# Performance work log

Hardware: AMD Instinct MI355X
Metric: run time of the kernel (lower is better)

## Reference

```python
import jax, jax.numpy as jnp
import numpy as np

D = 128        # node_state_dim
F = 10         # len(CHOSEN_CONNECTION_FEATURES)
N_IP = 20000
N_CONN = 100000
E = 200000
T = 3


def _seg_mean(vals, ids, n):
    s = jax.ops.segment_sum(vals, ids, num_segments=n)
    c = jax.ops.segment_sum(jnp.ones((vals.shape[0], 1), vals.dtype), ids, num_segments=n)
    return s / jnp.maximum(c, 1.0)


def _gru(x, h, kernel, rec_kernel, bias):
    # keras GRUCell, reset_after=True, gate order [z, r, hh]
    xm = x @ kernel + bias[0]
    hm = h @ rec_kernel + bias[1]
    xz, xr, xh = jnp.split(xm, 3, axis=-1)
    hz, hr, hh = jnp.split(hm, 3, axis=-1)
    z = jax.nn.sigmoid(xz + hz)
    r = jax.nn.sigmoid(xr + hr)
    hcand = jnp.tanh(xh + r * hh)
    return z * h + (1.0 - z) * hcand


def setup_inputs() -> dict:
    key = jax.random.key(0)
    ks = jax.random.split(key, 24)
    s = 0.02
    inp = {
        "feature_connection": jax.random.normal(ks[0], (N_CONN, F), jnp.float32),
        "src_ip_to_connection": jax.random.randint(ks[1], (E,), 0, N_IP, jnp.int32),
        "dst_ip_to_connection": jax.random.randint(ks[2], (E,), 0, N_CONN, jnp.int32),
        "src_connection_to_ip": jax.random.randint(ks[3], (E,), 0, N_CONN, jnp.int32),
        "dst_connection_to_ip": jax.random.randint(ks[4], (E,), 0, N_IP, jnp.int32),
        # message MLPs
        "W_m1": jax.random.normal(ks[5], (2 * D, D), jnp.float32) * s,
        "b_m1": jnp.zeros((D,), jnp.float32),
        "W_m2": jax.random.normal(ks[6], (2 * D, D), jnp.float32) * s,
        "b_m2": jnp.zeros((D,), jnp.float32),
        # GRU cells
        "gru_ip_k": jax.random.normal(ks[7], (D, 3 * D), jnp.float32) * s,
        "gru_ip_r": jax.random.normal(ks[8], (D, 3 * D), jnp.float32) * s,
        "gru_ip_b": jnp.zeros((2, 3 * D), jnp.float32),
        "gru_c_k": jax.random.normal(ks[9], (D, 3 * D), jnp.float32) * s,
        "gru_c_r": jax.random.normal(ks[10], (D, 3 * D), jnp.float32) * s,
        "gru_c_b": jnp.zeros((2, 3 * D), jnp.float32),
        # readout MLP
        "W_r1": jax.random.normal(ks[11], (D, 128), jnp.float32) * s,
        "b_r1": jnp.zeros((128,), jnp.float32),
        "W_r2": jax.random.normal(ks[12], (128, 64), jnp.float32) * s,
        "b_r2": jnp.zeros((64,), jnp.float32),
        "W_r3": jax.random.normal(ks[13], (64, 15), jnp.float32) * s,
        "b_r3": jnp.zeros((15,), jnp.float32),
    }
    return inp


def reference(feature_connection, src_ip_to_connection, dst_ip_to_connection,
              src_connection_to_ip, dst_connection_to_ip,
              W_m1, b_m1, W_m2, b_m2,
              gru_ip_k, gru_ip_r, gru_ip_b,
              gru_c_k, gru_c_r, gru_c_b,
              W_r1, b_r1, W_r2, b_r2, W_r3, b_r3):
    ip_state = jnp.ones((N_IP, D), jnp.float32)
    connection_state = jnp.concatenate(
        [feature_connection, jnp.zeros((N_CONN, D - F), jnp.float32)], axis=1)

    for _ in range(T):
        # ip -> connection messages
        nn_in = jnp.concatenate([ip_state[src_ip_to_connection],
                                 connection_state[dst_ip_to_connection]], axis=1)
        ip_message = jax.nn.relu(nn_in @ W_m1 + b_m1)            # [E, D]
        ip_mean = _seg_mean(ip_message, dst_ip_to_connection, N_CONN)
        # connection -> ip messages
        nn_in2 = jnp.concatenate([connection_state[src_connection_to_ip],
                                  ip_state[dst_connection_to_ip]], axis=1)
        conn_message = jax.nn.relu(nn_in2 @ W_m2 + b_m2)         # [E, D]
        conn_mean = _seg_mean(conn_message, dst_connection_to_ip, N_IP)
        # GRU updates
        ip_state = _gru(conn_mean, ip_state, gru_ip_k, gru_ip_r, gru_ip_b)
        connection_state = _gru(ip_mean, connection_state, gru_c_k, gru_c_r, gru_c_b)

    h = jax.nn.relu(connection_state @ W_r1 + b_r1)
    h = jax.nn.relu(h @ W_r2 + b_r2)
    return jax.nn.softmax(h @ W_r3 + b_r3, axis=-1)              # [N_CONN, 15]
```

## Files before the change

kernel.cpp:

```cpp
#include <hip/hip_runtime.h>
#include <math.h>

#define D 128
#define NF 10
#define N_IP 20000
#define N_CONN 100000
#define NE 200000
#define T_ROUNDS 3

typedef unsigned short u16;
using bf16x8 = __attribute__((ext_vector_type(8))) short;
using floatx4 = __attribute__((ext_vector_type(4))) float;

__device__ inline u16 f2bf(float f) {
  union { float f; unsigned u; } v; v.f = f;
  unsigned u = v.u;
  return (u16)((u + 0x7fffu + ((u >> 16) & 1u)) >> 16);
}
__device__ inline float bf2f(u16 h) {
  union { unsigned u; float f; } v; v.u = ((unsigned)h) << 16; return v.f;
}
__device__ __forceinline__ unsigned cvtpk(float lo, float hi) {
  unsigned r;
  asm("v_cvt_pk_bf16_f32 %0, %1, %2" : "=v"(r) : "v"(lo), "v"(hi));
  return r;
}

__device__ inline float fsigmoid(float s) { return 1.f / (1.f + __expf(-s)); }
__device__ inline float ftanh(float a) {
  a = fminf(fmaxf(a, -15.f), 15.f);
  float e = __expf(2.f * a);
  return (e - 1.f) / (e + 1.f);
}

__device__ __forceinline__ void gld16(const u16* g, u16* l) {
  __builtin_amdgcn_global_load_lds(
      (const __attribute__((address_space(1))) unsigned int*)g,
      (__attribute__((address_space(3))) unsigned int*)l, 16, 0, 0);
}

__global__ void k_setup(u16* __restrict__ ip_state, u16* __restrict__ conn_state,
                        const float* __restrict__ feat, int* __restrict__ cnt,
                        const float* __restrict__ gik, const float* __restrict__ gir,
                        const float* __restrict__ gck, const float* __restrict__ gcr,
                        const float* __restrict__ Wm1, const float* __restrict__ Wm2,
                        const float* __restrict__ Wr1, const float* __restrict__ Wr2,
                        u16* __restrict__ gikb, u16* __restrict__ girb,
                        u16* __restrict__ gckb, u16* __restrict__ gcrb,
                        u16* __restrict__ wm1b, u16* __restrict__ wm2b,
                        u16* __restrict__ wm1t, u16* __restrict__ wm2t,
                        u16* __restrict__ wr1b, u16* __restrict__ wr2b,
                        float* __restrict__ csum, int* __restrict__ gctr) {
  int i = blockIdx.x * blockDim.x + threadIdx.x;
  const int nip = N_IP * D;
  const int nstate = (N_IP + N_CONN) * D;
  if (i < nip) {
    ip_state[i] = 0x3F80;
  } else if (i < nstate) {
    int j = i - nip;
    int r = j >> 7, c = j & 127;
    conn_state[j] = (c < NF) ? f2bf(feat[r * NF + c]) : (u16)0;
  }
  if (i < N_CONN + N_IP) cnt[i] = 0;
  if (i < 2) gctr[i] = 0;
  if (i < 196608) {
    int m = i / 49152, r = i % 49152;
    const float* W = (m == 0) ? gik : (m == 1) ? gir : (m == 2) ? gck : gcr;
    u16* Wb = (m == 0) ? gikb : (m == 1) ? girb : (m == 2) ? gckb : gcrb;
    int col = r >> 7, k = r & 127;
    Wb[r] = f2bf(W[k * 384 + col]);
  } else if (i < 278528) {
    int j = i - 196608;
    int m = j / 16384, r = j % 16384;
    const float* W; u16* Wb; int k0;
    if (m == 0) { W = Wm1; Wb = wm1b; k0 = 128; }
    else if (m == 1) { W = Wm2; Wb = wm2b; k0 = 128; }
    else if (m == 2) { W = Wm1; Wb = wm1t; k0 = 0; }
    else if (m == 3) { W = Wm2; Wb = wm2t; k0 = 0; }
    else { W = Wr1; Wb = wr1b; k0 = 0; }
    int col = r >> 7, k = r & 127;
    Wb[r] = f2bf(W[(k0 + k) * 128 + col]);
  } else if (i < 286720) {
    int r = i - 278528;
    int col = r >> 7, k = r & 127;
    wr2b[r] = f2bf(Wr2[k * 64 + col]);
  } else if (i < 286848) {
    int c = i - 286720;
    float s = 0.f;
    for (int k = 0; k < 128; k++) s += Wm1[k * 128 + c];
    csum[c] = s;
  }
}

__global__ void k_initP_count(const float* __restrict__ csum, const float* __restrict__ feat,
                              const float* __restrict__ Wm2,
                              u16* __restrict__ P1, u16* __restrict__ P2,
                              const int* __restrict__ d1, const int* __restrict__ d2,
                              int* __restrict__ c1, int* __restrict__ c2) {
  int i = blockIdx.x * blockDim.x + threadIdx.x;
  if (i < NE) {
    atomicAdd(&c1[d1[i]], 1);
    atomicAdd(&c2[d2[i]], 1);
  }
  const int n1 = N_IP * 16;
  const int n2 = N_CONN * 16;
  if (i < n1) {
    int r = i >> 4, g = i & 15;
    u16 v[8];
#pragma unroll
    for (int k = 0; k < 8; k++) v[k] = f2bf(csum[g * 8 + k]);
    *(uint4*)(P1 + (size_t)r * 128 + g * 8) = *(const uint4*)v;
  } else if (i < n1 + n2) {
    int j = i - n1;
    int r = j >> 4, g = j & 15;
    float acc[8] = {0.f, 0.f, 0.f, 0.f, 0.f, 0.f, 0.f, 0.f};
#pragma unroll
    for (int k = 0; k < NF; k++) {
      float f = feat[(size_t)r * NF + k];
      const float* wrow = Wm2 + (size_t)k * 128 + g * 8;
#pragma unroll
      for (int c = 0; c < 8; c++) acc[c] += f * wrow[c];
    }
    u16 v[8];
#pragma unroll
    for (int c = 0; c < 8; c++) v[c] = f2bf(acc[c]);
    *(uint4*)(P2 + (size_t)r * 128 + g * 8) = *(const uint4*)v;
  }
}

__global__ void k_alloc(const int* __restrict__ cnt1, int* __restrict__ off1,
                        int* __restrict__ cur1, int n1, int nb1,
                        const int* __restrict__ cnt2, int* __restrict__ off2,
                        int* __restrict__ cur2, int n2, int* __restrict__ gctr) {
  const int* cnt; int* off; int* cur; int n, b; int* g;
  if ((int)blockIdx.x < nb1) {
    cnt = cnt1; off = off1; cur = cur1; n = n1; b = blockIdx.x; g = gctr;
  } else {
    cnt = cnt2; off = off2; cur = cur2; n = n2; b = blockIdx.x - nb1; g = gctr + 1;
  }
  int t = threadIdx.x;
  int base = b * 1024 + t * 4;
  int vals[4]; int s = 0;
#pragma unroll
  for (int i = 0; i < 4; i++) {
    int j = base + i;
    vals[i] = (j < n) ? cnt[j] : 0;
    s += vals[i];
  }
  int lane = t & 63, wv = t >> 6;
  int x = s;
  for (int d = 1; d < 64; d <<= 1) { int y = __shfl_up(x, d, 64); if (lane >= d) x += y; }
  __shared__ int wsum[4];
  __shared__ int gbase;
  if (lane == 63) wsum[wv] = x;
  __syncthreads();
  int add = 0;
  for (int i = 0; i < wv; i++) add += wsum[i];
  if (t == 0) gbase = atomicAdd(g, wsum[0] + wsum[1] + wsum[2] + wsum[3]);
  __syncthreads();
  int run = gbase + add + x - s;
#pragma unroll
  for (int i = 0; i < 4; i++) {
    int j = base + i;
    if (j < n) { off[j] = run; cur[j] = run; }
    run += vals[i];
  }
}

__global__ void k_scatter(const int* __restrict__ s1, const int* __restrict__ d1,
                          const int* __restrict__ s2, const int* __restrict__ d2,
                          int* __restrict__ cur1, int* __restrict__ cur2,
                          int* __restrict__ o1, int* __restrict__ o2) {
  int e = blockIdx.x * blockDim.x + threadIdx.x;
  if (e >= NE) return;
  int p1 = atomicAdd(&cur1[d1[e]], 1);
  o1[p1] = s1[e];
  int p2 = atomicAdd(&cur2[d2[e]], 1);
  o2[p2] = s2[e];
}

__global__ __launch_bounds__(512, 4) void k_msggru(
    u16* __restrict__ st1, const u16* __restrict__ wq1, const float* __restrict__ qb1,
    const u16* __restrict__ P1g, const int* __restrict__ srcs1g,
    const int* __restrict__ off1g, const int* __restrict__ cnt1g,
    const u16* __restrict__ wx1, const u16* __restrict__ wh1, const float* __restrict__ gb1,
    const u16* __restrict__ wp1, u16* __restrict__ Pn1, int r1, int tiles1,
    u16* __restrict__ st2, const u16* __restrict__ wq2, const float* __restrict__ qb2,
    const u16* __restrict__ P2g, const int* __restrict__ srcs2g,
    const int* __restrict__ off2g, const int* __restrict__ cnt2g,
    const u16* __restrict__ wx2, const u16* __restrict__ wh2, const float* __restrict__ gb2,
    const u16* __restrict__ wp2, u16* __restrict__ Pn2, int r2, int doP,
    const u16* __restrict__ w1r, const float* __restrict__ b1r,
    const u16* __restrict__ w2r, const float* __restrict__ b2r,
    const float* __restrict__ W3r, const float* __restrict__ b3r,
    float* __restrict__ outp, int doRd) {
  __shared__ __align__(16) char smem[65536];
  u16* Wls = (u16*)smem;
  u16* Qb = (u16*)smem;
  u16* bufA = (u16*)smem;
  u16* bufB = (u16*)(smem + 12288);
  u16* Hls = (u16*)(smem + 32768);
  u16* H; const u16* Wqb; const float* qbias; const u16* P;
  const int* srcs; const int* off; const int* cnt;
  const u16* Wxb; const u16* Whb; const float* gbias;
  const u16* Wpt; u16* Pn; int rows, bm;
  const bool side2 = (int)blockIdx.x >= tiles1;
  if (!side2) {
    H = st1; Wqb = wq1; qbias = qb1; P = P1g; srcs = srcs1g; off = off1g; cnt = cnt1g;
    Wxb = wx1; Whb = wh1; gbias = gb1; Wpt = wp1; Pn = Pn1; rows = r1; bm = blockIdx.x * 128;
  } else {
    H = st2; Wqb = wq2; qbias = qb2; P = P2g; srcs = srcs2g; off = off2g; cnt = cnt2g;
    Wxb = wx2; Whb = wh2; gbias = gb2; Wpt = wp2; Pn = Pn2; rows = r2;
    bm = (blockIdx.x - tiles1) * 128;
  }
  const int tid = threadIdx.x, wv = tid >> 6, lane = tid & 63;
  const int lrow = lane & 15, quad = lane >> 4;
#pragma unroll
  for (int j = 0; j < 4; j++) {
    int c = j * 512 + tid;
    int row = c >> 4, sl = c & 15;
    gld16(Wqb + (size_t)row * 128 + ((sl ^ (row & 15)) * 8), Wls + (size_t)c * 8);
  }
#pragma unroll
  for (int i = 0; i < 4; i++) {
    int c = i * 512 + tid;
    int row = c >> 4, sl = c & 15;
    gld16(H + (size_t)(bm + row) * 128 + ((sl ^ (row & 15)) * 8), Hls + (size_t)c * 8);
  }
  int oArr[4], nArr[4];
#pragma unroll
  for (int it = 0; it < 4; it++) {
    int nl = (it * 512 + tid) >> 4;
    int node = bm + nl;
    oArr[it] = (node < rows) ? off[node] : 0;
    nArr[it] = (node < rows) ? cnt[node] : 0;
  }
  __syncthreads();
  bf16x8 ah[4];
#pragma unroll
  for (int ks = 0; ks < 4; ks++)
    ah[ks] = *(const bf16x8*)(Hls + (size_t)(wv * 16 + lrow) * 128 + (((ks * 4 + quad) ^ lrow) * 8));
  floatx4 acc[8];
#pragma unroll
  for (int ct = 0; ct < 8; ct++) acc[ct] = {0.f, 0.f, 0.f, 0.f};
#pragma unroll
  for (int ks = 0; ks < 4; ks++) {
#pragma unroll
    for (int ct = 0; ct < 8; ct++) {
      bf16x8 b = *(const bf16x8*)(Wls + (size_t)(ct * 16 + lrow) * 128 + (((4 * ks + quad) ^ lrow) * 8));
      acc[ct] = __builtin_amdgcn_mfma_f32_16x16x32_bf16(ah[ks], b, acc[ct], 0, 0, 0);
    }
  }
  __syncthreads();
  {
    const int lr = wv * 16 + quad * 4;
#pragma unroll
    for (int ct = 0; ct < 8; ct++) {
      int col = ct * 16 + lrow;
      float bv = qbias[col];
      unsigned p01 = cvtpk(acc[ct][0] + bv, acc[ct][1] + bv);
      unsigned p23 = cvtpk(acc[ct][2] + bv, acc[ct][3] + bv);
      Qb[(size_t)(lr + 0) * 128 + col] = (u16)p01;
      Qb[(size_t)(lr + 1) * 128 + col] = (u16)(p01 >> 16);
      Qb[(size_t)(lr + 2) * 128 + col] = (u16)p23;
      Qb[(size_t)(lr + 3) * 128 + col] = (u16)(p23 >> 16);
    }
  }
  __syncthreads();
#pragma unroll
  for (int it = 0; it < 4; it++) {
    int task = it * 512 + tid;
    int nl = task >> 4, g = task & 15;
    int node = bm + nl;
    if (node >= rows) continue;
    int c8 = g << 3;
    float q[8];
    {
      uint4 qv = *(const uint4*)(Qb + (size_t)nl * 128 + c8);
      unsigned qq[4] = {qv.x, qv.y, qv.z, qv.w};
#pragma unroll
      for (int k = 0; k < 4; k++) {
        q[2 * k] = __uint_as_float(qq[k] << 16);
        q[2 * k + 1] = __uint_as_float(qq[k] & 0xffff0000u);
      }
    }
    float acg[8] = {0.f, 0.f, 0.f, 0.f, 0.f, 0.f, 0.f, 0.f};
    int o = oArr[it], n = nArr[it];
    for (int i = 0; i < n; i += 4) {
      int rem = n - i;
      int s0 = srcs[o + i];
      int s1 = srcs[o + i + (rem > 1 ? 1 : 0)];
      int s2 = srcs[o + i + (rem > 2 ? 2 : 0)];
      int s3 = srcs[o + i + (rem > 3 ? 3 : 0)];
      uint4 v0 = *(const uint4*)(P + (size_t)s0 * 128 + c8);
      uint4 v1 = *(const uint4*)(P + (size_t)s1 * 128 + c8);
      uint4 v2 = *(const uint4*)(P + (size_t)s2 * 128 + c8);
      uint4 v3 = *(const uint4*)(P + (size_t)s3 * 128 + c8);
      unsigned w[16] = {v0.x, v0.y, v0.z, v0.w, v1.x, v1.y, v1.z, v1.w,
                        v2.x, v2.y, v2.z, v2.w, v3.x, v3.y, v3.z, v3.w};
#pragma unroll
      for (int e = 0; e < 4; e++) {
        bool val = (e == 0) || (rem > e);
#pragma unroll
        for (int k = 0; k < 4; k++) {
          unsigned ww = w[e * 4 + k];
          float lo = __uint_as_float(ww << 16);
          float hi = __uint_as_float(ww & 0xffff0000u);
          float t0 = fmaxf(lo + q[2 * k], 0.f);
          float t1 = fmaxf(hi + q[2 * k + 1], 0.f);
          if (val) { acg[2 * k] += t0; acg[2 * k + 1] += t1; }
        }
      }
    }
    float inv = 1.f / fmaxf((float)n, 1.f);
    uint4 ov;
    ov.x = cvtpk(acg[0] * inv, acg[1] * inv);
    ov.y = cvtpk(acg[2] * inv, acg[3] * inv);
    ov.z = cvtpk(acg[4] * inv, acg[5] * inv);
    ov.w = cvtpk(acg[6] * inv, acg[7] * inv);
    *(uint4*)(Qb + (size_t)nl * 128 + ((g ^ (nl & 15)) * 8)) = ov;
  }
  __syncthreads();
  bf16x8 ax[4];
#pragma unroll
  for (int ks = 0; ks < 4; ks++)
    ax[ks] = *(const bf16x8*)(Qb + (size_t)(wv * 16 + lrow) * 128 + (((ks * 4 + quad) ^ lrow) * 8));
  const int lr0 = wv * 16 + quad * 4;
  __syncthreads();
#pragma unroll
  for (int j = 0; j < 2; j++) {
    int c = j * 512 + tid;
    if (c < 768) {
      int gate = c >> 8, colw = (c >> 4) & 15, sl = c & 15;
      gld16(Wxb + (size_t)(gate * 128 + 0 * 16 + colw) * 128 + ((sl ^ colw) * 8),
            bufA + (size_t)c * 8);
    }
  }
  for (int ch = 0; ch < 8; ch++) {
    __syncthreads();
#pragma unroll
    for (int j = 0; j < 2; j++) {
      int c = j * 512 + tid;
      if (c < 768) {
        int gate = c >> 8, colw = (c >> 4) & 15, sl = c & 15;
        gld16(Whb + (size_t)(gate * 128 + ch * 16 + colw) * 128 + ((sl ^ colw) * 8),
              bufB + (size_t)c * 8);
      }
    }
    floatx4 gacc[3][2];
#pragma unroll
    for (int g = 0; g < 3; g++) {
      gacc[g][0] = {0.f, 0.f, 0.f, 0.f};
      gacc[g][1] = {0.f, 0.f, 0.f, 0.f};
    }
#pragma unroll
    for (int ks = 0; ks < 4; ks++) {
      int posu = ((4 * ks + quad) ^ lrow) * 8;
#pragma unroll
      for (int g = 0; g < 3; g++) {
        bf16x8 bx = *(const bf16x8*)(bufA + (size_t)(g * 16 + lrow) * 128 + posu);
        gacc[g][0] = __builtin_amdgcn_mfma_f32_16x16x32_bf16(ax[ks], bx, gacc[g][0], 0, 0, 0);
      }
    }
    __syncthreads();
    if (ch < 7) {
#pragma unroll
      for (int j = 0; j < 2; j++) {
        int c = j * 512 + tid;
        if (c < 768) {
          int gate = c >> 8, colw = (c >> 4) & 15, sl = c & 15;
          gld16(Wxb + (size_t)(gate * 128 + (ch + 1) * 16 + colw) * 128 + ((sl ^ colw) * 8),
                bufA + (size_t)c * 8);
        }
      }
    }
#pragma unroll
    for (int ks = 0; ks < 4; ks++) {
      int posu = ((4 * ks + quad) ^ lrow) * 8;
#pragma unroll
      for (int g = 0; g < 3; g++) {
        bf16x8 bh = *(const bf16x8*)(bufB + (size_t)(g * 16 + lrow) * 128 + posu);
        gacc[g][1] = __builtin_amdgcn_mfma_f32_16x16x32_bf16(ah[ks], bh, gacc[g][1], 0, 0, 0);
      }
    }
    int hcol = ch * 16 + lrow;
    float bxz = gbias[hcol];
    float bxr = gbias[128 + hcol];
    float bxh = gbias[256 + hcol];
    float bhz = gbias[384 + hcol];
    float bhr = gbias[384 + 128 + hcol];
    float bhh = gbias[384 + 256 + hcol];
    int ggr = 2 * ch + (lrow >> 3);
    int gel = lrow & 7;
    float hn[4];
#pragma unroll
    for (int reg = 0; reg < 4; reg++) {
      int lr = lr0 + reg;
      float xz = gacc[0][0][reg] + bxz;
      float xr = gacc[1][0][reg] + bxr;
      float xh = gacc[2][0][reg] + bxh;
      float hz = gacc[0][1][reg] + bhz;
      float hr = gacc[1][1][reg] + bhr;
      float hh = gacc[2][1][reg] + bhh;
      float z = fsigmoid(xz + hz);
      float rr = fsigmoid(xr + hr);
      float hc = ftanh(xh + rr * hh);
      const u16* hp = Hls + (size_t)lr * 128 + ((ggr ^ (lr & 15)) * 8) + gel;
      float hold = bf2f(*hp);
      hn[reg] = z * hold + (1.f - z) * hc;
    }
    unsigned q01 = cvtpk(hn[0], hn[1]);
    unsigned q23 = cvtpk(hn[2], hn[3]);
#define HPTR(R) (Hls + (size_t)(lr0 + (R)) * 128 + ((ggr ^ ((lr0 + (R)) & 15)) * 8) + gel)
    *HPTR(0) = (u16)q01;
    *HPTR(1) = (u16)(q01 >> 16);
    *HPTR(2) = (u16)q23;
    *HPTR(3) = (u16)(q23 >> 16);
#undef HPTR
  }
  __syncthreads();
  if (!doRd) {
#pragma unroll
    for (int i = 0; i < 4; i++) {
      int c = i * 512 + tid;
      int row = c >> 4, g = c & 15;
      int grow = bm + row;
      if (grow < rows)
        *(uint4*)(H + (size_t)grow * 128 + g * 8) =
            *(const uint4*)(Hls + (size_t)row * 128 + ((g ^ (row & 15)) * 8));
    }
  }
  if (doP) {
    bf16x8 ah2[4];
#pragma unroll
    for (int ks = 0; ks < 4; ks++)
      ah2[ks] = *(const bf16x8*)(Hls + (size_t)(wv * 16 + lrow) * 128 + (((ks * 4 + quad) ^ lrow) * 8));
#pragma unroll
    for (int j = 0; j < 4; j++) {
      int c = j * 512 + tid;
      int row = c >> 4, sl = c & 15;
      gld16(Wpt + (size_t)row * 128 + ((sl ^ (row & 15)) * 8), Wls + (size_t)c * 8);
    }
    __syncthreads();
#pragma unroll
    for (int ct = 0; ct < 8; ct++) acc[ct] = {0.f, 0.f, 0.f, 0.f};
#pragma unroll
    for (int ks = 0; ks < 4; ks++) {
#pragma unroll
      for (int ct = 0; ct < 8; ct++) {
        bf16x8 b = *(const bf16x8*)(Wls + (size_t)(ct * 16 + lrow) * 128 + (((4 * ks + quad) ^ lrow) * 8));
        acc[ct] = __builtin_amdgcn_mfma_f32_16x16x32_bf16(ah2[ks], b, acc[ct], 0, 0, 0);
      }
    }
    u16* Cls = Hls;
    {
      const int lr = wv * 16 + quad * 4;
#pragma unroll
      for (int ct = 0; ct < 8; ct++) {
        int col = ct * 16 + lrow;
        unsigned p01 = cvtpk(acc[ct][0], acc[ct][1]);
        unsigned p23 = cvtpk(acc[ct][2], acc[ct][3]);
        Cls[(size_t)(lr + 0) * 128 + col] = (u16)p01;
        Cls[(size_t)(lr + 1) * 128 + col] = (u16)(p01 >> 16);
        Cls[(size_t)(lr + 2) * 128 + col] = (u16)p23;
        Cls[(size_t)(lr + 3) * 128 + col] = (u16)(p23 >> 16);
      }
    }
    __syncthreads();
#pragma unroll
    for (int i = 0; i < 4; i++) {
      int c = i * 512 + tid;
      int row = c >> 4, g = c & 15;
      int grow = bm + row;
      if (grow < rows)
        *(uint4*)(Pn + (size_t)grow * 128 + g * 8) =
            *(const uint4*)(Cls + (size_t)row * 128 + g * 8);
    }
    return;
  }
  if (!doRd || !side2) return;
  bf16x8 ar[4];
#pragma unroll
  for (int ks = 0; ks < 4; ks++)
    ar[ks] = *(const bf16x8*)(Hls + (size_t)(wv * 16 + lrow) * 128 + (((ks * 4 + quad) ^ lrow) * 8));
#pragma unroll
  for (int j = 0; j < 4; j++) {
    int c = j * 512 + tid;
    int row = c >> 4, sl = c & 15;
    gld16(w1r + (size_t)row * 128 + ((sl ^ (row & 15)) * 8), Wls + (size_t)c * 8);
  }
  __syncthreads();
#pragma unroll
  for (int ct = 0; ct < 8; ct++) acc[ct] = {0.f, 0.f, 0.f, 0.f};
#pragma unroll
  for (int ks = 0; ks < 4; ks++) {
#pragma unroll
    for (int ct = 0; ct < 8; ct++) {
      bf16x8 b = *(const bf16x8*)(Wls + (size_t)(ct * 16 + lrow) * 128 + (((4 * ks + quad) ^ lrow) * 8));
      acc[ct] = __builtin_amdgcn_mfma_f32_16x16x32_bf16(ar[ks], b, acc[ct], 0, 0, 0);
    }
  }
#pragma unroll
  for (int ct = 0; ct < 8; ct++) {
    int col = ct * 16 + lrow;
    float bv = b1r[col];
    int ggr = 2 * ct + (lrow >> 3);
    int gel = lrow & 7;
    unsigned p01 = cvtpk(fmaxf(acc[ct][0] + bv, 0.f), fmaxf(acc[ct][1] + bv, 0.f));
    unsigned p23 = cvtpk(fmaxf(acc[ct][2] + bv, 0.f), fmaxf(acc[ct][3] + bv, 0.f));
#define H1PTR(R) (Hls + (size_t)(lr0 + (R)) * 128 + ((ggr ^ ((lr0 + (R)) & 15)) * 8) + gel)
    *H1PTR(0) = (u16)p01;
    *H1PTR(1) = (u16)(p01 >> 16);
    *H1PTR(2) = (u16)p23;
    *H1PTR(3) = (u16)(p23 >> 16);
#undef H1PTR
  }
  __syncthreads();
#pragma unroll
  for (int j = 0; j < 2; j++) {
    int c = j * 512 + tid;
    int row = c >> 4, sl = c & 15;
    gld16(w2r + (size_t)row * 128 + ((sl ^ (row & 15)) * 8), Wls + (size_t)c * 8);
  }
  __syncthreads();
  bf16x8 a2[4];
#pragma unroll
  for (int ks = 0; ks < 4; ks++)
    a2[ks] = *(const bf16x8*)(Hls + (size_t)(wv * 16 + lrow) * 128 + (((ks * 4 + quad) ^ lrow) * 8));
  floatx4 acc2[4];
#pragma unroll
  for (int ct = 0; ct < 4; ct++) acc2[ct] = {0.f, 0.f, 0.f, 0.f};
#pragma unroll
  for (int ks = 0; ks < 4; ks++) {
#pragma unroll
    for (int ct = 0; ct < 4; ct++) {
      bf16x8 b = *(const bf16x8*)(Wls + (size_t)(ct * 16 + lrow) * 128 + (((4 * ks + quad) ^ lrow) * 8));
      acc2[ct] = __builtin_amdgcn_mfma_f32_16x16x32_bf16(a2[ks], b, acc2[ct], 0, 0, 0);
    }
  }
  __syncthreads();
  u16* H2 = (u16*)smem;
  float* W3ls = (float*)(smem + 18432);
  float* b3ls = (float*)(smem + 18432 + 3840);
#pragma unroll
  for (int ct = 0; ct < 4; ct++) {
    int col = ct * 16 + lrow;
    float bv = b2r[col];
#pragma unroll
    for (int reg = 0; reg < 4; reg++)
      H2[(size_t)(lr0 + reg) * 72 + col] = f2bf(fmaxf(acc2[ct][reg] + bv, 0.f));
  }
  for (int l = tid; l < 960; l += 512) W3ls[l] = W3r[l];
  if (tid < 15) b3ls[tid] = b3r[tid];
  __syncthreads();
  {
    int col = tid & 15;
    int rb = (tid >> 4) * 4;
    float lg[4] = {0.f, 0.f, 0.f, 0.f};
    if (col < 15) {
      float b3v = b3ls[col];
      lg[0] = b3v; lg[1] = b3v; lg[2] = b3v; lg[3] = b3v;
      for (int k8 = 0; k8 < 64; k8 += 8) {
        float w[8];
#pragma unroll
        for (int j = 0; j < 8; j++) w[j] = W3ls[(k8 + j) * 15 + col];
#pragma unroll
        for (int r = 0; r < 4; r++) {
          bf16x8 hv = *(const bf16x8*)(H2 + (size_t)(rb + r) * 72 + k8);
#pragma unroll
          for (int j = 0; j < 8; j++) lg[r] += bf2f((u16)hv[j]) * w[j];
        }
      }
    }
#pragma unroll
    for (int r = 0; r < 4; r++) {
      float v = (col < 15) ? lg[r] : -3.0e38f;
      float m = v;
#pragma unroll
      for (int d = 1; d < 16; d <<= 1) m = fmaxf(m, __shfl_xor(m, d, 16));
      float e = (col < 15) ? __expf(lg[r] - m) : 0.f;
      float s = e;
#pragma unroll
      for (int d = 1; d < 16; d <<= 1) s += __shfl_xor(s, d, 16);
      int gr2 = bm + rb + r;
      if (col < 15 && gr2 < rows) outp[(size_t)gr2 * 15 + col] = e / s;
    }
  }
}

extern "C" void kernel_launch(void* const* d_in, const int* in_sizes, int n_in,
                              void* d_out, int out_size, void* d_ws, size_t ws_size,
                              hipStream_t stream) {
  const float* feat = (const float*)d_in[0];
  const int* src1 = (const int*)d_in[1];
  const int* dst1 = (const int*)d_in[2];
  const int* src2 = (const int*)d_in[3];
  const int* dst2 = (const int*)d_in[4];
  const float* Wm1 = (const float*)d_in[5];
  const float* bm1 = (const float*)d_in[6];
  const float* Wm2 = (const float*)d_in[7];
  const float* bm2 = (const float*)d_in[8];
  const float* gik = (const float*)d_in[9];
  const float* gir = (const float*)d_in[10];
  const float* gib = (const float*)d_in[11];
  const float* gck = (const float*)d_in[12];
  const float* gcr = (const float*)d_in[13];
  const float* gcb = (const float*)d_in[14];
  const float* Wr1 = (const float*)d_in[15];
  const float* br1 = (const float*)d_in[16];
  const float* Wr2 = (const float*)d_in[17];
  const float* br2 = (const float*)d_in[18];
  const float* Wr3 = (const float*)d_in[19];
  const float* br3 = (const float*)d_in[20];
  float* out = (float*)d_out;

  u16* w16 = (u16*)d_ws;
  size_t o = 0;
  u16* ip_state = w16 + o;   o += (size_t)N_IP * D;
  u16* conn_state = w16 + o; o += (size_t)N_CONN * D;
  u16* P1a = w16 + o;        o += (size_t)N_IP * D;
  u16* P2a = w16 + o;        o += (size_t)N_CONN * D;
  u16* P1b = w16 + o;        o += (size_t)N_IP * D;
  u16* P2b = w16 + o;        o += (size_t)N_CONN * D;
  u16* gikb = w16 + o;       o += 49152;
  u16* girb = w16 + o;       o += 49152;
  u16* gckb = w16 + o;       o += 49152;
  u16* gcrb = w16 + o;       o += 49152;
  u16* wm1b = w16 + o;       o += 16384;
  u16* wm2b = w16 + o;       o += 16384;
  u16* wm1t = w16 + o;       o += 16384;
  u16* wm2t = w16 + o;       o += 16384;
  u16* wr1b = w16 + o;       o += 16384;
  u16* wr2b = w16 + o;       o += 8192;
  float* csum = (float*)(w16 + o); o += 256;
  int* ip = (int*)(w16 + o);
  int* cnt1 = ip;  ip += N_CONN;
  int* cnt2 = ip;  ip += N_IP;
  int* off1 = ip;  ip += N_CONN;
  int* off2 = ip;  ip += N_IP;
  int* cur1 = ip;  ip += N_CONN;
  int* cur2 = ip;  ip += N_IP;
  int* srcs1 = ip; ip += NE;
  int* srcs2 = ip; ip += NE;
  int* gctr = ip;  ip += 8;

  const int BT = 256;

  const int nstate = (N_IP + N_CONN) * D;
  k_setup<<<(nstate + BT - 1) / BT, BT, 0, stream>>>(
      ip_state, conn_state, feat, cnt1,
      gik, gir, gck, gcr, Wm1, Wm2, Wr1, Wr2,
      gikb, girb, gckb, gcrb, wm1b, wm2b, wm1t, wm2t, wr1b, wr2b, csum, gctr);
  const int nPinit = (N_IP + N_CONN) * 16;
  k_initP_count<<<(nPinit + BT - 1) / BT, BT, 0, stream>>>(
      csum, feat, Wm2, P1a, P2a, dst1, dst2, cnt1, cnt2);

  const int nb1 = (N_CONN + 1023) / 1024, nb2 = (N_IP + 1023) / 1024;
  k_alloc<<<nb1 + nb2, 256, 0, stream>>>(cnt1, off1, cur1, N_CONN, nb1,
                                         cnt2, off2, cur2, N_IP, gctr);
  k_scatter<<<(NE + BT - 1) / BT, BT, 0, stream>>>(src1, dst1, src2, dst2,
                                                   cur1, cur2, srcs1, srcs2);

  const int t128ip = (N_IP + 127) / 128;
  const int t128cn = (N_CONN + 127) / 128;

  u16* P1buf[2] = {P1a, P1b};
  u16* P2buf[2] = {P2a, P2b};
  for (int t = 0; t < T_ROUNDS; t++) {
    int cu = t & 1, nx = cu ^ 1;
    int last = (t == T_ROUNDS - 1);
    int grid = last ? t128cn : (t128ip + t128cn);
    int tiles1 = last ? 0 : t128ip;
    k_msggru<<<grid, 512, 0, stream>>>(
        ip_state, wm2b, bm2, P2buf[cu], srcs2, off2, cnt2, gikb, girb, gib,
        wm1t, P1buf[nx], N_IP, tiles1,
        conn_state, wm1b, bm1, P1buf[cu], srcs1, off1, cnt1, gckb, gcrb, gcb,
        wm2t, P2buf[nx], N_CONN, last ? 0 : 1,
        wr1b, br1, wr2b, br2, Wr3, br3, out, last ? 1 : 0);
  }
}
```

Baseline: 431.0 us.

## Synthesize initial states in round zero instead of materializing them in setup

The initial ip state (all ones) and connection state (features padded with zeros) are no longer written to global memory in setup. Round 0 of the fused message/GRU kernel builds them on the fly: ip rows use constant ones registers, and connection rows are filled in LDS from the feature array. Because every initial ip row is identical, the projected ip message P1 is the same for all rows, so the round-0 aggregation for connections skips the gather and multiplies a single precomputed relu value by the edge count. This removes large state and P1 initialization writes and the round-0 gather traffic, in exchange for extra branches in the main kernel.

```diff
diff --git a/kernel.cpp b/kernel.cpp
--- a/kernel.cpp
+++ b/kernel.cpp
@@ -39,9 +39,7 @@
       (__attribute__((address_space(3))) unsigned int*)l, 16, 0, 0);
 }
 
-__global__ void k_setup(u16* __restrict__ ip_state, u16* __restrict__ conn_state,
-                        const float* __restrict__ feat, int* __restrict__ cnt,
-                        const float* __restrict__ gik, const float* __restrict__ gir,
+__global__ void k_setup(const float* __restrict__ gik, const float* __restrict__ gir,
                         const float* __restrict__ gck, const float* __restrict__ gcr,
                         const float* __restrict__ Wm1, const float* __restrict__ Wm2,
                         const float* __restrict__ Wr1, const float* __restrict__ Wr2,
@@ -50,17 +48,9 @@
                         u16* __restrict__ wm1b, u16* __restrict__ wm2b,
                         u16* __restrict__ wm1t, u16* __restrict__ wm2t,
                         u16* __restrict__ wr1b, u16* __restrict__ wr2b,
-                        float* __restrict__ csum, int* __restrict__ gctr) {
+                        float* __restrict__ csum, int* __restrict__ cnt,
+                        int* __restrict__ gctr) {
   int i = blockIdx.x * blockDim.x + threadIdx.x;
-  const int nip = N_IP * D;
-  const int nstate = (N_IP + N_CONN) * D;
-  if (i < nip) {
-    ip_state[i] = 0x3F80;
-  } else if (i < nstate) {
-    int j = i - nip;
-    int r = j >> 7, c = j & 127;
-    conn_state[j] = (c < NF) ? f2bf(feat[r * NF + c]) : (u16)0;
-  }
   if (i < N_CONN + N_IP) cnt[i] = 0;
   if (i < 2) gctr[i] = 0;
   if (i < 196608) {
@@ -92,9 +82,8 @@
   }
 }
 
-__global__ void k_initP_count(const float* __restrict__ csum, const float* __restrict__ feat,
-                              const float* __restrict__ Wm2,
-                              u16* __restrict__ P1, u16* __restrict__ P2,
+__global__ void k_initP_count(const float* __restrict__ feat, const float* __restrict__ Wm2,
+                              u16* __restrict__ P2,
                               const int* __restrict__ d1, const int* __restrict__ d2,
                               int* __restrict__ c1, int* __restrict__ c2) {
   int i = blockIdx.x * blockDim.x + threadIdx.x;
@@ -102,17 +91,8 @@
     atomicAdd(&c1[d1[i]], 1);
     atomicAdd(&c2[d2[i]], 1);
   }
-  const int n1 = N_IP * 16;
-  const int n2 = N_CONN * 16;
-  if (i < n1) {
+  if (i < N_CONN * 16) {
     int r = i >> 4, g = i & 15;
-    u16 v[8];
-#pragma unroll
-    for (int k = 0; k < 8; k++) v[k] = f2bf(csum[g * 8 + k]);
-    *(uint4*)(P1 + (size_t)r * 128 + g * 8) = *(const uint4*)v;
-  } else if (i < n1 + n2) {
-    int j = i - n1;
-    int r = j >> 4, g = j & 15;
     float acc[8] = {0.f, 0.f, 0.f, 0.f, 0.f, 0.f, 0.f, 0.f};
 #pragma unroll
     for (int k = 0; k < NF; k++) {
@@ -193,7 +173,8 @@
     const u16* __restrict__ w1r, const float* __restrict__ b1r,
     const u16* __restrict__ w2r, const float* __restrict__ b2r,
     const float* __restrict__ W3r, const float* __restrict__ b3r,
-    float* __restrict__ outp, int doRd) {
+    float* __restrict__ outp, int doRd,
+    const float* __restrict__ featp, const float* __restrict__ csumP, int an0) {
   __shared__ __align__(16) char smem[65536];
   u16* Wls = (u16*)smem;
   u16* Qb = (u16*)smem;
@@ -215,17 +196,35 @@
   }
   const int tid = threadIdx.x, wv = tid >> 6, lane = tid & 63;
   const int lrow = lane & 15, quad = lane >> 4;
+  const bool anIp = an0 && !side2;
+  const bool anConn = an0 && side2;
 #pragma unroll
   for (int j = 0; j < 4; j++) {
     int c = j * 512 + tid;
     int row = c >> 4, sl = c & 15;
     gld16(Wqb + (size_t)row * 128 + ((sl ^ (row & 15)) * 8), Wls + (size_t)c * 8);
   }
-#pragma unroll
-  for (int i = 0; i < 4; i++) {
-    int c = i * 512 + tid;
-    int row = c >> 4, sl = c & 15;
-    gld16(H + (size_t)(bm + row) * 128 + ((sl ^ (row & 15)) * 8), Hls + (size_t)c * 8);
+  if (!an0) {
+#pragma unroll
+    for (int i = 0; i < 4; i++) {
+      int c = i * 512 + tid;
+      int row = c >> 4, sl = c & 15;
+      gld16(H + (size_t)(bm + row) * 128 + ((sl ^ (row & 15)) * 8), Hls + (size_t)c * 8);
+    }
+  } else if (anConn) {
+#pragma unroll
+    for (int i = 0; i < 4; i++) {
+      int c = i * 512 + tid;
+      int row = c >> 4, sl = c & 15;
+      int grow = bm + row;
+      u16 v[8];
+#pragma unroll
+      for (int k = 0; k < 8; k++) {
+        int col = sl * 8 + k;
+        v[k] = (grow < rows && col < NF) ? f2bf(featp[(size_t)grow * NF + col]) : (u16)0;
+      }
+      *(uint4*)(Hls + (size_t)row * 128 + ((sl ^ (row & 15)) * 8)) = *(const uint4*)v;
+    }
   }
   int oArr[4], nArr[4];
 #pragma unroll
@@ -237,9 +236,17 @@
   }
   __syncthreads();
   bf16x8 ah[4];
-#pragma unroll
-  for (int ks = 0; ks < 4; ks++)
-    ah[ks] = *(const bf16x8*)(Hls + (size_t)(wv * 16 + lrow) * 128 + (((ks * 4 + quad) ^ lrow) * 8));
+  if (anIp) {
+    bf16x8 ones;
+#pragma unroll
+    for (int k = 0; k < 8; k++) ones[k] = (short)0x3F80;
+#pragma unroll
+    for (int ks = 0; ks < 4; ks++) ah[ks] = ones;
+  } else {
+#pragma unroll
+    for (int ks = 0; ks < 4; ks++)
+      ah[ks] = *(const bf16x8*)(Hls + (size_t)(wv * 16 + lrow) * 128 + (((ks * 4 + quad) ^ lrow) * 8));
+  }
   floatx4 acc[8];
 #pragma unroll
   for (int ct = 0; ct < 8; ct++) acc[ct] = {0.f, 0.f, 0.f, 0.f};
@@ -285,30 +292,42 @@
       }
     }
     float acg[8] = {0.f, 0.f, 0.f, 0.f, 0.f, 0.f, 0.f, 0.f};
-    int o = oArr[it], n = nArr[it];
-    for (int i = 0; i < n; i += 4) {
-      int rem = n - i;
-      int s0 = srcs[o + i];
-      int s1 = srcs[o + i + (rem > 1 ? 1 : 0)];
-      int s2 = srcs[o + i + (rem > 2 ? 2 : 0)];
-      int s3 = srcs[o + i + (rem > 3 ? 3 : 0)];
-      uint4 v0 = *(const uint4*)(P + (size_t)s0 * 128 + c8);
-      uint4 v1 = *(const uint4*)(P + (size_t)s1 * 128 + c8);
-      uint4 v2 = *(const uint4*)(P + (size_t)s2 * 128 + c8);
-      uint4 v3 = *(const uint4*)(P + (size_t)s3 * 128 + c8);
-      unsigned w[16] = {v0.x, v0.y, v0.z, v0.w, v1.x, v1.y, v1.z, v1.w,
-                        v2.x, v2.y, v2.z, v2.w, v3.x, v3.y, v3.z, v3.w};
-#pragma unroll
-      for (int e = 0; e < 4; e++) {
-        bool val = (e == 0) || (rem > e);
-#pragma unroll
-        for (int k = 0; k < 4; k++) {
-          unsigned ww = w[e * 4 + k];
-          float lo = __uint_as_float(ww << 16);
-          float hi = __uint_as_float(ww & 0xffff0000u);
-          float t0 = fmaxf(lo + q[2 * k], 0.f);
-          float t1 = fmaxf(hi + q[2 * k + 1], 0.f);
-          if (val) { acg[2 * k] += t0; acg[2 * k + 1] += t1; }
+    int n = nArr[it];
+    if (anConn) {
+      float t[8];
+#pragma unroll
+      for (int k = 0; k < 8; k++)
+        t[k] = fmaxf(bf2f(f2bf(csumP[c8 + k])) + q[k], 0.f);
+      for (int i = 0; i < n; i++) {
+#pragma unroll
+        for (int k = 0; k < 8; k++) acg[k] += t[k];
+      }
+    } else {
+      int o = oArr[it];
+      for (int i = 0; i < n; i += 4) {
+        int rem = n - i;
+        int s0 = srcs[o + i];
+        int s1 = srcs[o + i + (rem > 1 ? 1 : 0)];
+        int s2 = srcs[o + i + (rem > 2 ? 2 : 0)];
+        int s3 = srcs[o + i + (rem > 3 ? 3 : 0)];
+        uint4 v0 = *(const uint4*)(P + (size_t)s0 * 128 + c8);
+        uint4 v1 = *(const uint4*)(P + (size_t)s1 * 128 + c8);
+        uint4 v2 = *(const uint4*)(P + (size_t)s2 * 128 + c8);
+        uint4 v3 = *(const uint4*)(P + (size_t)s3 * 128 + c8);
+        unsigned w[16] = {v0.x, v0.y, v0.z, v0.w, v1.x, v1.y, v1.z, v1.w,
+                          v2.x, v2.y, v2.z, v2.w, v3.x, v3.y, v3.z, v3.w};
+#pragma unroll
+        for (int e = 0; e < 4; e++) {
+          bool val = (e == 0) || (rem > e);
+#pragma unroll
+          for (int k = 0; k < 4; k++) {
+            unsigned ww = w[e * 4 + k];
+            float lo = __uint_as_float(ww << 16);
+            float hi = __uint_as_float(ww & 0xffff0000u);
+            float t0 = fmaxf(lo + q[2 * k], 0.f);
+            float t1 = fmaxf(hi + q[2 * k + 1], 0.f);
+            if (val) { acg[2 * k] += t0; acg[2 * k + 1] += t1; }
+          }
         }
       }
     }
@@ -405,8 +424,13 @@
       float z = fsigmoid(xz + hz);
       float rr = fsigmoid(xr + hr);
       float hc = ftanh(xh + rr * hh);
-      const u16* hp = Hls + (size_t)lr * 128 + ((ggr ^ (lr & 15)) * 8) + gel;
-      float hold = bf2f(*hp);
+      float hold;
+      if (anIp) {
+        hold = 1.0f;
+      } else {
+        const u16* hp = Hls + (size_t)lr * 128 + ((ggr ^ (lr & 15)) * 8) + gel;
+        hold = bf2f(*hp);
+      }
       hn[reg] = z * hold + (1.f - z) * hc;
     }
     unsigned q01 = cvtpk(hn[0], hn[1]);
@@ -646,14 +670,11 @@
 
   const int BT = 256;
 
-  const int nstate = (N_IP + N_CONN) * D;
-  k_setup<<<(nstate + BT - 1) / BT, BT, 0, stream>>>(
-      ip_state, conn_state, feat, cnt1,
+  k_setup<<<(286848 + BT - 1) / BT, BT, 0, stream>>>(
       gik, gir, gck, gcr, Wm1, Wm2, Wr1, Wr2,
-      gikb, girb, gckb, gcrb, wm1b, wm2b, wm1t, wm2t, wr1b, wr2b, csum, gctr);
-  const int nPinit = (N_IP + N_CONN) * 16;
-  k_initP_count<<<(nPinit + BT - 1) / BT, BT, 0, stream>>>(
-      csum, feat, Wm2, P1a, P2a, dst1, dst2, cnt1, cnt2);
+      gikb, girb, gckb, gcrb, wm1b, wm2b, wm1t, wm2t, wr1b, wr2b, csum, cnt1, gctr);
+  k_initP_count<<<(N_CONN * 16 + BT - 1) / BT, BT, 0, stream>>>(
+      feat, Wm2, P2a, dst1, dst2, cnt1, cnt2);
 
   const int nb1 = (N_CONN + 1023) / 1024, nb2 = (N_IP + 1023) / 1024;
   k_alloc<<<nb1 + nb2, 256, 0, stream>>>(cnt1, off1, cur1, N_CONN, nb1,
@@ -676,6 +697,7 @@
         wm1t, P1buf[nx], N_IP, tiles1,
         conn_state, wm1b, bm1, P1buf[cu], srcs1, off1, cnt1, gckb, gcrb, gcb,
         wm2t, P2buf[nx], N_CONN, last ? 0 : 1,
-        wr1b, br1, wr2b, br2, Wr3, br3, out, last ? 1 : 0);
-  }
-}
+        wr1b, br1, wr2b, br2, Wr3, br3, out, last ? 1 : 0,
+        feat, csum, (t == 0) ? 1 : 0);
+  }
+}
```

After: 420.3 us. -2.5%, faster.
